# Kernel optimization log

Hardware: AMD Instinct MI355X
Metric: run time of the kernel (lower is better)

## Reference

```python
import jax, jax.numpy as jnp
import numpy as np

KERNEL = 4  # conv kernel_size == stride


def setup_inputs() -> dict:
    key = jax.random.key(0)
    k1, k2, k3, k4 = jax.random.split(key, 4)
    x = jax.random.normal(k1, (16, 3, 512, 512), dtype=jnp.float32)
    w_sample = jax.random.normal(k2, (64, 3, KERNEL, KERNEL), dtype=jnp.float32) * 0.1
    b_sample = jax.random.normal(k3, (64,), dtype=jnp.float32) * 0.1
    centers = jax.random.uniform(k4, (8,), dtype=jnp.float32)
    return {"x": x, "w_sample": w_sample, "b_sample": b_sample, "centers": centers}


def _spectral_normalize(w):
    # torch spectral_norm divides the weight by its top singular value
    # (estimated by power iteration; we compute it exactly, same math at convergence)
    wm = w.reshape(w.shape[0], -1)  # [out, in*kh*kw]
    sigma = jnp.linalg.svd(wm, compute_uv=False)[0]
    return w / sigma


def _forward(x, w_sample, b_sample, centers):
    wn = _spectral_normalize(w_sample)
    # strided conv: 3 -> C channels, kernel=stride=4, no padding  -> [B,C,H/4,W/4]
    y = jax.lax.conv_general_dilated(
        x, wn, window_strides=(KERNEL, KERNEL), padding='VALID',
        dimension_numbers=('NCHW', 'OIHW', 'NCHW'))
    y = y + b_sample[None, :, None, None]
    # soft VQ: squared distance to each center, softmax(-dist)-weighted sum of centers
    quant_dist = (y[..., None] - centers) ** 2          # [B,C,H',W',K]
    soft = jnp.sum(centers * jax.nn.softmax(-quant_dist, axis=-1), axis=-1)
    return soft


def reference(x, w_sample, b_sample, centers):
    return _forward(x, w_sample, b_sample, centers)
```

## Files before the change

kernel.cpp:

```cpp
#include <hip/hip_runtime.h>
#include <stdint.h>

#define CIN 3
#define WW 512
#define HW (512 * 512)
#define COUT 64
#define KF 48
#define HO 128
#define WO 128
#define LDA 52

#define NTAB 2048
#define YMIN (-12.0f)
#define YMAX (12.0f)
#define INVH ((float)NTAB / (YMAX - YMIN))
#define WS_TAB_OFF 128
#define WS_FLOATS (WS_TAB_OFF + 2 * NTAB)

typedef __attribute__((ext_vector_type(8))) short short8;
typedef __attribute__((ext_vector_type(4))) float f32x4;

union FragU { uint32_t u[4]; short8 s; };

__device__ __forceinline__ uint32_t pack_bf16_pair(float f0, float f1) {
  return (__float_as_uint(f0) >> 16) | (__float_as_uint(f1) & 0xffff0000u);
}
__device__ __forceinline__ float trunc_bf16f(float f) {
  return __uint_as_float(__float_as_uint(f) & 0xffff0000u);
}
__device__ __forceinline__ void split_pair(float4 a, float4 b, short8& hi, short8& lo) {
  FragU h, l;
  h.u[0] = pack_bf16_pair(a.x, a.y);
  h.u[1] = pack_bf16_pair(a.z, a.w);
  h.u[2] = pack_bf16_pair(b.x, b.y);
  h.u[3] = pack_bf16_pair(b.z, b.w);
  l.u[0] = pack_bf16_pair(a.x - trunc_bf16f(a.x), a.y - trunc_bf16f(a.y));
  l.u[1] = pack_bf16_pair(a.z - trunc_bf16f(a.z), a.w - trunc_bf16f(a.w));
  l.u[2] = pack_bf16_pair(b.x - trunc_bf16f(b.x), b.y - trunc_bf16f(b.y));
  l.u[3] = pack_bf16_pair(b.z - trunc_bf16f(b.z), b.w - trunc_bf16f(b.w));
  hi = h.s; lo = l.s;
}

__device__ __forceinline__ float vq_eval(float y, const float* __restrict__ c) {
  float d[8], m;
#pragma unroll
  for (int k = 0; k < 8; ++k) { float t = y - c[k]; d[k] = t * t; }
  m = fminf(fminf(fminf(d[0], d[1]), fminf(d[2], d[3])),
            fminf(fminf(d[4], d[5]), fminf(d[6], d[7])));
  float num = 0.f, den = 0.f;
#pragma unroll
  for (int k = 0; k < 8; ++k) {
    float e = __expf(m - d[k]);
    den += e;
    num = fmaf(c[k], e, num);
  }
  return num / den;
}

__global__ __launch_bounds__(256) void prep_sigma(
    const float* __restrict__ w, const float* __restrict__ bias,
    const float* __restrict__ centers, float* __restrict__ ws) {
  const int t = threadIdx.x;

  if (blockIdx.x == 1) {
    float c[8];
#pragma unroll
    for (int k = 0; k < 8; ++k) c[k] = centers[k];
    const float h = (YMAX - YMIN) / (float)NTAB;
#pragma unroll 1
    for (int k = t; k < NTAB; k += 256) {
      float y0 = YMIN + (float)k * h;
      float f0 = vq_eval(y0, c);
      float f1 = vq_eval(y0 + h, c);
      ws[WS_TAB_OFF + 2 * k]     = f0;
      ws[WS_TAB_OFF + 2 * k + 1] = f1 - f0;
    }
    if (t < COUT) ws[2 + t] = (bias[t] - YMIN) * INVH;
    return;
  }

  __shared__ float sW[COUT * KF];
  __shared__ float sG[KF * LDA];
  __shared__ float sA[KF * LDA];
  __shared__ float sB[KF * LDA];
  __shared__ float sv[64];
  __shared__ float sp[256];

  {
    const float4* w4 = (const float4*)w;
    float4* s4 = (float4*)sW;
#pragma unroll
    for (int q = 0; q < 3; ++q) s4[q * 256 + t] = w4[q * 256 + t];
  }
  __syncthreads();

  const int ti = t >> 4, tj = t & 15;
  const int i0 = 3 * ti, j0 = 3 * tj;
  {
    float acc[3][3] = {{0.f}};
#pragma unroll 4
    for (int m = 0; m < COUT; ++m) {
      const float* wr = sW + m * KF;
      float a0 = wr[i0], a1 = wr[i0 + 1], a2 = wr[i0 + 2];
      float b0 = wr[j0], b1 = wr[j0 + 1], b2 = wr[j0 + 2];
      acc[0][0] = fmaf(a0, b0, acc[0][0]);
      acc[0][1] = fmaf(a0, b1, acc[0][1]);
      acc[0][2] = fmaf(a0, b2, acc[0][2]);
      acc[1][0] = fmaf(a1, b0, acc[1][0]);
      acc[1][1] = fmaf(a1, b1, acc[1][1]);
      acc[1][2] = fmaf(a1, b2, acc[1][2]);
      acc[2][0] = fmaf(a2, b0, acc[2][0]);
      acc[2][1] = fmaf(a2, b1, acc[2][1]);
      acc[2][2] = fmaf(a2, b2, acc[2][2]);
    }
#pragma unroll
    for (int ii = 0; ii < 3; ++ii)
#pragma unroll
      for (int jj = 0; jj < 3; ++jj) {
        sG[(i0 + ii) * LDA + j0 + jj] = acc[ii][jj];
        sA[(i0 + ii) * LDA + j0 + jj] = acc[ii][jj];
      }
  }
  __syncthreads();

#pragma unroll 1
  for (int s = 0; s < 4; ++s) {
    const float* src = (s & 1) ? sB : sA;
    float* dst = (s & 1) ? sA : sB;
    float acc[3][3] = {{0.f}};
#pragma unroll
    for (int q = 0; q < 12; ++q) {
      float4 ar0 = *(const float4*)(src + (i0 + 0) * LDA + 4 * q);
      float4 ar1 = *(const float4*)(src + (i0 + 1) * LDA + 4 * q);
      float4 ar2 = *(const float4*)(src + (i0 + 2) * LDA + 4 * q);
      float4 br0 = *(const float4*)(src + (j0 + 0) * LDA + 4 * q);
      float4 br1 = *(const float4*)(src + (j0 + 1) * LDA + 4 * q);
      float4 br2 = *(const float4*)(src + (j0 + 2) * LDA + 4 * q);
#define DOT4(A, B, C) \
      C = fmaf(A.x, B.x, C); C = fmaf(A.y, B.y, C); \
      C = fmaf(A.z, B.z, C); C = fmaf(A.w, B.w, C);
      DOT4(ar0, br0, acc[0][0]); DOT4(ar0, br1, acc[0][1]); DOT4(ar0, br2, acc[0][2]);
      DOT4(ar1, br0, acc[1][0]); DOT4(ar1, br1, acc[1][1]); DOT4(ar1, br2, acc[1][2]);
      DOT4(ar2, br0, acc[2][0]); DOT4(ar2, br1, acc[2][1]); DOT4(ar2, br2, acc[2][2]);
#undef DOT4
    }
    __syncthreads();
#pragma unroll
    for (int ii = 0; ii < 3; ++ii)
#pragma unroll
      for (int jj = 0; jj < 3; ++jj)
        dst[(i0 + ii) * LDA + j0 + jj] = acc[ii][jj];
    __syncthreads();
  }
  const float* M = sA;

  if (t < 64) sv[t] = (t < KF) ? 1.0f : 0.f;
  __syncthreads();

#pragma unroll 1
  for (int it = 0; it < 6; ++it) {
    float partial = 0.f;
    if (t < 192) {
      const int row = t >> 2, seg = t & 3;
      const float* mr = M + row * LDA + seg * 12;
      const float4* v4 = (const float4*)sv;
#pragma unroll
      for (int q = 0; q < 3; ++q) {
        float4 m4 = *(const float4*)(mr + 4 * q);
        float4 vv = v4[seg * 3 + q];
        partial = fmaf(m4.x, vv.x, partial);
        partial = fmaf(m4.y, vv.y, partial);
        partial = fmaf(m4.z, vv.z, partial);
        partial = fmaf(m4.w, vv.w, partial);
      }
    }
    sp[t] = partial;
    __syncthreads();
    if (t < 64) {
      float nv = 0.f;
      if (t < KF) nv = (sp[4 * t] + sp[4 * t + 1]) + (sp[4 * t + 2] + sp[4 * t + 3]);
      float ss = nv * nv;
#pragma unroll
      for (int m = 32; m >= 1; m >>= 1) ss += __shfl_xor(ss, m, 64);
      sv[t] = (t < KF) ? nv * rsqrtf(ss) : 0.f;
    }
    __syncthreads();
  }

  {
    float partial = 0.f;
    if (t < 192) {
      const int row = t >> 2, seg = t & 3;
      const float* mr = sG + row * LDA + seg * 12;
      const float4* v4 = (const float4*)sv;
#pragma unroll
      for (int q = 0; q < 3; ++q) {
        float4 m4 = *(const float4*)(mr + 4 * q);
        float4 vv = v4[seg * 3 + q];
        partial = fmaf(m4.x, vv.x, partial);
        partial = fmaf(m4.y, vv.y, partial);
        partial = fmaf(m4.z, vv.z, partial);
        partial = fmaf(m4.w, vv.w, partial);
      }
    }
    sp[t] = partial;
    __syncthreads();
    if (t < 64) {
      float nv = 0.f;
      if (t < KF) nv = (sp[4 * t] + sp[4 * t + 1]) + (sp[4 * t + 2] + sp[4 * t + 3]);
      float vt = sv[t];
      float num = nv * vt;
      float den = vt * vt;
#pragma unroll
      for (int m = 32; m >= 1; m >>= 1) {
        num += __shfl_xor(num, m, 64);
        den += __shfl_xor(den, m, 64);
      }
      if (t == 0) {
        float sg = sqrtf(num / den);
        ws[0] = sg;
        ws[1] = INVH / sg;
      }
    }
  }
}

__global__ __launch_bounds__(256) void conv_vq_mfma(
    const float* __restrict__ x, const float* __restrict__ w,
    const float* __restrict__ params, float* __restrict__ out) {
  __shared__ float stab[2 * NTAB];
  __shared__ float so[COUT];
  const int t = threadIdx.x;
  {
    const float4* src = (const float4*)(params + WS_TAB_OFF);
    float4* dst = (float4*)stab;
#pragma unroll
    for (int q = 0; q < 4; ++q) dst[q * 256 + t] = src[q * 256 + t];
    if (t < COUT) so[t] = params[2 + t];
  }
  __syncthreads();

  const float a_scale = params[1];

  const int lane = t & 63;
  const int wv   = t >> 6;
  const int g    = lane >> 4;
  const int nl   = lane & 15;

  const int n0   = blockIdx.x * 128 + wv * 32;
  const int b    = n0 >> 14;
  const int rem0 = n0 & 16383;
  const int i    = rem0 >> 7;
  const int j0   = rem0 & 127;

  const float* xb = x + (size_t)b * (CIN * HW) + (size_t)(4 * i) * WW;
  const short8 zfrag = {0, 0, 0, 0, 0, 0, 0, 0};

  short8 Bh[2][2], Bl[2][2];
#pragma unroll
  for (int s = 0; s < 2; ++s) {
    const float* base = xb + 4 * (j0 + s * 16 + nl);
    {
      const int ci = g >> 1, kh = (g & 1) * 2;
      float4 fa = *(const float4*)(base + (size_t)ci * HW + kh * WW);
      float4 fb = *(const float4*)(base + (size_t)ci * HW + (kh + 1) * WW);
      split_pair(fa, fb, Bh[s][0], Bl[s][0]);
    }
    if (g < 2) {
      const int kh = g * 2;
      float4 fa = *(const float4*)(base + (size_t)2 * HW + kh * WW);
      float4 fb = *(const float4*)(base + (size_t)2 * HW + (kh + 1) * WW);
      split_pair(fa, fb, Bh[s][1], Bl[s][1]);
    } else {
      Bh[s][1] = zfrag; Bl[s][1] = zfrag;
    }
  }

  const float2* tab2 = (const float2*)stab;
  float* opb = out + (size_t)b * (COUT * 16384) + (size_t)(i * 128 + j0);

#pragma unroll 2
  for (int m = 0; m < 4; ++m) {
    const float* wr = w + (size_t)(m * 16 + nl) * KF;
    short8 Ah[2], Al[2];
    {
      float4 fa = *(const float4*)(wr + 8 * g);
      float4 fb = *(const float4*)(wr + 8 * g + 4);
      split_pair(fa, fb, Ah[0], Al[0]);
    }
    if (g < 2) {
      float4 fa = *(const float4*)(wr + 32 + 8 * g);
      float4 fb = *(const float4*)(wr + 36 + 8 * g);
      split_pair(fa, fb, Ah[1], Al[1]);
    } else {
      Ah[1] = zfrag; Al[1] = zfrag;
    }

#pragma unroll
    for (int s = 0; s < 2; ++s) {
      f32x4 acc = {0.f, 0.f, 0.f, 0.f};
      acc = __builtin_amdgcn_mfma_f32_16x16x32_bf16(Ah[0], Bh[s][0], acc, 0, 0, 0);
      acc = __builtin_amdgcn_mfma_f32_16x16x32_bf16(Ah[1], Bh[s][1], acc, 0, 0, 0);
      acc = __builtin_amdgcn_mfma_f32_16x16x32_bf16(Ah[0], Bl[s][0], acc, 0, 0, 0);
      acc = __builtin_amdgcn_mfma_f32_16x16x32_bf16(Al[0], Bh[s][0], acc, 0, 0, 0);
      acc = __builtin_amdgcn_mfma_f32_16x16x32_bf16(Ah[1], Bl[s][1], acc, 0, 0, 0);
      acc = __builtin_amdgcn_mfma_f32_16x16x32_bf16(Al[1], Bh[s][1], acc, 0, 0, 0);

      float* op = opb + s * 16 + nl;
#pragma unroll
      for (int r = 0; r < 4; ++r) {
        const int ch = m * 16 + 4 * g + r;
        float u = fmaf(acc[r], a_scale, so[ch]);
        u = fmaxf(u, 0.0f);
        u = fminf(u, (float)NTAB - 0.0005f);
        const int k = (int)u;
        const float fr = u - (float)k;
        const float2 e = tab2[k];
        op[(size_t)ch * 16384] = fmaf(fr, e.y, e.x);
      }
    }
  }
}

__global__ __launch_bounds__(256) void conv_vq_exp(
    const float* __restrict__ x, const float* __restrict__ w,
    const float* __restrict__ bias, const float* __restrict__ centers,
    const float* __restrict__ sigma_ptr, float* __restrict__ out) {
  const int t = threadIdx.x;
  const int pos = blockIdx.x * 256 + t;
  const int b   = pos >> 14;
  const int rem = pos & 16383;
  const int i   = rem >> 7;
  const int j   = rem & 127;

  const float inv_sigma = 1.0f / sigma_ptr[0];
  float cc[8], tc[8], mc2[8];
#pragma unroll
  for (int k = 0; k < 8; ++k) {
    float c = centers[k];
    cc[k] = c; tc[k] = 2.0f * c; mc2[k] = -c * c;
  }
  const float* xp = x + (size_t)b * (CIN * HW) + (size_t)(4 * i) * WW + 4 * j;
  float p[KF];
#pragma unroll
  for (int ci = 0; ci < CIN; ++ci)
#pragma unroll
    for (int kh = 0; kh < 4; ++kh) {
      float4 v4 = *(const float4*)(xp + (size_t)ci * HW + kh * WW);
      p[(ci * 4 + kh) * 4 + 0] = v4.x;
      p[(ci * 4 + kh) * 4 + 1] = v4.y;
      p[(ci * 4 + kh) * 4 + 2] = v4.z;
      p[(ci * 4 + kh) * 4 + 3] = v4.w;
    }
  float* op = out + (size_t)b * (COUT * HO * WO) + rem;
#pragma unroll 2
  for (int c = 0; c < COUT; ++c) {
    const float4* wr = (const float4*)(w + c * KF);
    float a0 = 0.f, a1 = 0.f, a2 = 0.f, a3 = 0.f;
#pragma unroll
    for (int q = 0; q < 12; ++q) {
      float4 gq = wr[q];
      a0 = fmaf(p[4*q+0], gq.x, a0);
      a1 = fmaf(p[4*q+1], gq.y, a1);
      a2 = fmaf(p[4*q+2], gq.z, a2);
      a3 = fmaf(p[4*q+3], gq.w, a3);
    }
    const float y = fmaf((a0 + a1) + (a2 + a3), inv_sigma, bias[c]);
    float e0 = __expf(fmaf(tc[0], y, mc2[0])), e1 = __expf(fmaf(tc[1], y, mc2[1]));
    float e2 = __expf(fmaf(tc[2], y, mc2[2])), e3 = __expf(fmaf(tc[3], y, mc2[3]));
    float e4 = __expf(fmaf(tc[4], y, mc2[4])), e5 = __expf(fmaf(tc[5], y, mc2[5]));
    float e6 = __expf(fmaf(tc[6], y, mc2[6])), e7 = __expf(fmaf(tc[7], y, mc2[7]));
    float den = ((e0 + e1) + (e2 + e3)) + ((e4 + e5) + (e6 + e7));
    float num = (fmaf(cc[0], e0, cc[1] * e1) + fmaf(cc[2], e2, cc[3] * e3)) +
                (fmaf(cc[4], e4, cc[5] * e5) + fmaf(cc[6], e6, cc[7] * e7));
    op[(size_t)c * (HO * WO)] = __fdividef(num, den);
  }
}

extern "C" void kernel_launch(void* const* d_in, const int* in_sizes, int n_in,
                              void* d_out, int out_size, void* d_ws, size_t ws_size,
                              hipStream_t stream) {
  const float* x       = (const float*)d_in[0];
  const float* w       = (const float*)d_in[1];
  const float* b       = (const float*)d_in[2];
  const float* centers = (const float*)d_in[3];
  float* out = (float*)d_out;
  float* ws  = (float*)d_ws;

  const int use_table = (ws_size >= (size_t)WS_FLOATS * sizeof(float)) ? 1 : 0;

  prep_sigma<<<use_table ? 2 : 1, 256, 0, stream>>>(w, b, centers, ws);
  if (use_table)
    conv_vq_mfma<<<(16 * HO * WO) / 128, 256, 0, stream>>>(x, w, ws, out);
  else
    conv_vq_exp<<<(16 * HO * WO) / 256, 256, 0, stream>>>(x, w, b, centers, ws, out);
}
```

Before: 42.37 us.

## Use 32x32x16 MFMA with pre-split scaled weights and bias-initialised accumulators

The prep kernel now scales the weights by the table scale factor, splits them into bf16 hi/lo pairs and stores them in MFMA fragment layout in the workspace. The main kernel switches from 16x16x32 to 32x32x16 bf16 MFMA tiles with 64 pixels per block, each wave handling 32 channels by 32 pixels. Bias is loaded straight into the accumulator, which removes the per-weight split work and the scale FMA from the main kernel. In exchange the grid doubles and each block loads the 16 KB lookup table twice as often, and the workspace requirement grows.

After: 39.44 us. -6.9%, faster.

```diff
diff --git a/kernel.cpp b/kernel.cpp
--- a/kernel.cpp
+++ b/kernel.cpp
@@ -15,10 +15,12 @@
 #define YMAX (12.0f)
 #define INVH ((float)NTAB / (YMAX - YMIN))
 #define WS_TAB_OFF 128
-#define WS_FLOATS (WS_TAB_OFF + 2 * NTAB)
+#define WS_WP_HI 4352
+#define WS_WP_LO 5888
+#define WS_FLOATS (WS_WP_LO + 1536)
 
 typedef __attribute__((ext_vector_type(8))) short short8;
-typedef __attribute__((ext_vector_type(4))) float f32x4;
+typedef __attribute__((ext_vector_type(16))) float f32x16;
 
 union FragU { uint32_t u[4]; short8 s; };
 
@@ -59,7 +61,7 @@
 
 __global__ __launch_bounds__(256) void prep_sigma(
     const float* __restrict__ w, const float* __restrict__ bias,
-    const float* __restrict__ centers, float* __restrict__ ws) {
+    const float* __restrict__ centers, float* __restrict__ ws, int build_tab) {
   const int t = threadIdx.x;
 
   if (blockIdx.x == 1) {
@@ -85,6 +87,7 @@
   __shared__ float sB[KF * LDA];
   __shared__ float sv[64];
   __shared__ float sp[256];
+  __shared__ float s_a;
 
   {
     const float4* w4 = (const float4*)w;
@@ -220,105 +223,107 @@
         float sg = sqrtf(num / den);
         ws[0] = sg;
         ws[1] = INVH / sg;
+        s_a = INVH / sg;
       }
     }
   }
-}
-
-__global__ __launch_bounds__(256) void conv_vq_mfma(
-    const float* __restrict__ x, const float* __restrict__ w,
-    const float* __restrict__ params, float* __restrict__ out) {
+  __syncthreads();
+
+  if (build_tab) {
+    const float a = s_a;
+#pragma unroll 1
+    for (int slot = t; slot < 384; slot += 256) {
+      const int ct = slot / 192;
+      const int rm = slot % 192;
+      const int kk = rm >> 6;
+      const int l  = rm & 63;
+      const int row = ct * 32 + (l & 31);
+      const int kbase = kk * 16 + (l >> 5) * 8;
+      const float* src = w + row * KF + kbase;
+      float4 fa = *(const float4*)(src);
+      float4 fb = *(const float4*)(src + 4);
+      fa.x *= a; fa.y *= a; fa.z *= a; fa.w *= a;
+      fb.x *= a; fb.y *= a; fb.z *= a; fb.w *= a;
+      short8 hi, lo;
+      split_pair(fa, fb, hi, lo);
+      *(short8*)(ws + WS_WP_HI + slot * 4) = hi;
+      *(short8*)(ws + WS_WP_LO + slot * 4) = lo;
+    }
+  }
+}
+
+__global__ __launch_bounds__(256) void conv_vq_mfma2(
+    const float* __restrict__ x, const float* __restrict__ params,
+    float* __restrict__ out) {
   __shared__ float stab[2 * NTAB];
-  __shared__ float so[COUT];
+  __shared__ float sso[COUT];
   const int t = threadIdx.x;
   {
     const float4* src = (const float4*)(params + WS_TAB_OFF);
     float4* dst = (float4*)stab;
 #pragma unroll
     for (int q = 0; q < 4; ++q) dst[q * 256 + t] = src[q * 256 + t];
-    if (t < COUT) so[t] = params[2 + t];
+    if (t < COUT) sso[t] = params[2 + t];
   }
   __syncthreads();
-
-  const float a_scale = params[1];
 
   const int lane = t & 63;
   const int wv   = t >> 6;
-  const int g    = lane >> 4;
-  const int nl   = lane & 15;
-
-  const int n0   = blockIdx.x * 128 + wv * 32;
+  const int ct   = wv & 1;
+  const int pt   = wv >> 1;
+  const int h    = lane >> 5;
+  const int pl   = lane & 31;
+
+  const int n0   = blockIdx.x * 64;
   const int b    = n0 >> 14;
   const int rem0 = n0 & 16383;
   const int i    = rem0 >> 7;
-  const int j0   = rem0 & 127;
-
-  const float* xb = x + (size_t)b * (CIN * HW) + (size_t)(4 * i) * WW;
-  const short8 zfrag = {0, 0, 0, 0, 0, 0, 0, 0};
-
-  short8 Bh[2][2], Bl[2][2];
-#pragma unroll
-  for (int s = 0; s < 2; ++s) {
-    const float* base = xb + 4 * (j0 + s * 16 + nl);
-    {
-      const int ci = g >> 1, kh = (g & 1) * 2;
-      float4 fa = *(const float4*)(base + (size_t)ci * HW + kh * WW);
-      float4 fb = *(const float4*)(base + (size_t)ci * HW + (kh + 1) * WW);
-      split_pair(fa, fb, Bh[s][0], Bl[s][0]);
-    }
-    if (g < 2) {
-      const int kh = g * 2;
-      float4 fa = *(const float4*)(base + (size_t)2 * HW + kh * WW);
-      float4 fb = *(const float4*)(base + (size_t)2 * HW + (kh + 1) * WW);
-      split_pair(fa, fb, Bh[s][1], Bl[s][1]);
-    } else {
-      Bh[s][1] = zfrag; Bl[s][1] = zfrag;
-    }
+  const int jj   = (rem0 & 127) + pt * 32 + pl;
+
+  const float* xb = x + (size_t)b * (CIN * HW) + (size_t)(4 * i) * WW + 4 * jj;
+  float4 xf[3][2];
+#pragma unroll
+  for (int kk = 0; kk < 3; ++kk) {
+    xf[kk][0] = *(const float4*)(xb + (size_t)kk * HW + (2 * h) * WW);
+    xf[kk][1] = *(const float4*)(xb + (size_t)kk * HW + (2 * h + 1) * WW);
+  }
+  short8 Bh[3], Bl[3];
+#pragma unroll
+  for (int kk = 0; kk < 3; ++kk) split_pair(xf[kk][0], xf[kk][1], Bh[kk], Bl[kk]);
+
+  const short8* AhP = (const short8*)(params + WS_WP_HI) + ct * 192 + lane;
+  const short8* AlP = (const short8*)(params + WS_WP_LO) + ct * 192 + lane;
+  short8 Ah[3], Al[3];
+#pragma unroll
+  for (int kk = 0; kk < 3; ++kk) { Ah[kk] = AhP[kk * 64]; Al[kk] = AlP[kk * 64]; }
+
+  f32x16 acc;
+  {
+    const float* sob = sso + ct * 32 + 4 * h;
+#pragma unroll
+    for (int r = 0; r < 16; ++r) acc[r] = sob[(r & 3) + 8 * (r >> 2)];
+  }
+
+#pragma unroll
+  for (int kk = 0; kk < 3; ++kk)
+    acc = __builtin_amdgcn_mfma_f32_32x32x16_bf16(Ah[kk], Bh[kk], acc, 0, 0, 0);
+#pragma unroll
+  for (int kk = 0; kk < 3; ++kk) {
+    acc = __builtin_amdgcn_mfma_f32_32x32x16_bf16(Ah[kk], Bl[kk], acc, 0, 0, 0);
+    acc = __builtin_amdgcn_mfma_f32_32x32x16_bf16(Al[kk], Bh[kk], acc, 0, 0, 0);
   }
 
   const float2* tab2 = (const float2*)stab;
-  float* opb = out + (size_t)b * (COUT * 16384) + (size_t)(i * 128 + j0);
-
-#pragma unroll 2
-  for (int m = 0; m < 4; ++m) {
-    const float* wr = w + (size_t)(m * 16 + nl) * KF;
-    short8 Ah[2], Al[2];
-    {
-      float4 fa = *(const float4*)(wr + 8 * g);
-      float4 fb = *(const float4*)(wr + 8 * g + 4);
-      split_pair(fa, fb, Ah[0], Al[0]);
-    }
-    if (g < 2) {
-      float4 fa = *(const float4*)(wr + 32 + 8 * g);
-      float4 fb = *(const float4*)(wr + 36 + 8 * g);
-      split_pair(fa, fb, Ah[1], Al[1]);
-    } else {
-      Ah[1] = zfrag; Al[1] = zfrag;
-    }
-
-#pragma unroll
-    for (int s = 0; s < 2; ++s) {
-      f32x4 acc = {0.f, 0.f, 0.f, 0.f};
-      acc = __builtin_amdgcn_mfma_f32_16x16x32_bf16(Ah[0], Bh[s][0], acc, 0, 0, 0);
-      acc = __builtin_amdgcn_mfma_f32_16x16x32_bf16(Ah[1], Bh[s][1], acc, 0, 0, 0);
-      acc = __builtin_amdgcn_mfma_f32_16x16x32_bf16(Ah[0], Bl[s][0], acc, 0, 0, 0);
-      acc = __builtin_amdgcn_mfma_f32_16x16x32_bf16(Al[0], Bh[s][0], acc, 0, 0, 0);
-      acc = __builtin_amdgcn_mfma_f32_16x16x32_bf16(Ah[1], Bl[s][1], acc, 0, 0, 0);
-      acc = __builtin_amdgcn_mfma_f32_16x16x32_bf16(Al[1], Bh[s][1], acc, 0, 0, 0);
-
-      float* op = opb + s * 16 + nl;
-#pragma unroll
-      for (int r = 0; r < 4; ++r) {
-        const int ch = m * 16 + 4 * g + r;
-        float u = fmaf(acc[r], a_scale, so[ch]);
-        u = fmaxf(u, 0.0f);
-        u = fminf(u, (float)NTAB - 0.0005f);
-        const int k = (int)u;
-        const float fr = u - (float)k;
-        const float2 e = tab2[k];
-        op[(size_t)ch * 16384] = fmaf(fr, e.y, e.x);
-      }
-    }
+  float* ob = out + ((size_t)(b * COUT + ct * 32 + 4 * h)) * 16384 + i * 128 + jj;
+#pragma unroll
+  for (int r = 0; r < 16; ++r) {
+    float u = acc[r];
+    u = fmaxf(u, 0.0f);
+    u = fminf(u, (float)NTAB - 0.0005f);
+    const int k = (int)u;
+    const float fr = u - (float)k;
+    const float2 e = tab2[k];
+    ob[(size_t)((r & 3) + 8 * (r >> 2)) * 16384] = fmaf(fr, e.y, e.x);
   }
 }
 
@@ -389,9 +394,9 @@
 
   const int use_table = (ws_size >= (size_t)WS_FLOATS * sizeof(float)) ? 1 : 0;
 
-  prep_sigma<<<use_table ? 2 : 1, 256, 0, stream>>>(w, b, centers, ws);
+  prep_sigma<<<use_table ? 2 : 1, 256, 0, stream>>>(w, b, centers, ws, use_table);
   if (use_table)
-    conv_vq_mfma<<<(16 * HO * WO) / 128, 256, 0, stream>>>(x, w, ws, out);
+    conv_vq_mfma2<<<(16 * HO * WO) / 64, 256, 0, stream>>>(x, ws, out);
   else
     conv_vq_exp<<<(16 * HO * WO) / 256, 256, 0, stream>>>(x, w, b, centers, ws, out);
 }
```
